# Optimization experiments

Measured on AMD Instinct MI355X. Metric: run time of the kernel, lower is better.

## Reference

```python
import jax, jax.numpy as jnp
import numpy as np

N_NODES = 100000
N_EDGES = 1600000
N_CONCEPTS = 500000
D = 128  # concept_dim = graph_hidden_dim = graph_output_dim


def setup_inputs() -> dict:
    key = jax.random.key(0)
    ks = jax.random.split(key, 10)
    cncpt_ids = jax.random.randint(ks[0], (N_NODES,), 0, N_CONCEPTS)
    src = jax.random.randint(ks[1], (N_EDGES,), 0, N_NODES)
    dst = jax.random.randint(ks[2], (N_EDGES,), 0, N_NODES)
    emb_table = jax.random.normal(ks[3], (N_CONCEPTS, D), dtype=jnp.float32)
    W1 = jax.random.normal(ks[4], (D, D), dtype=jnp.float32) * 0.05
    b1 = jax.random.normal(ks[5], (D,), dtype=jnp.float32) * 0.05
    W2 = jax.random.normal(ks[6], (D, D), dtype=jnp.float32) * 0.05
    b2 = jax.random.normal(ks[7], (D,), dtype=jnp.float32) * 0.05
    Wout = jax.random.normal(ks[8], (1, D), dtype=jnp.float32) * 0.05
    bout = jax.random.normal(ks[9], (1,), dtype=jnp.float32) * 0.05
    return {"cncpt_ids": cncpt_ids, "src": src, "dst": dst,
            "emb_table": emb_table, "W1": W1, "b1": b1,
            "W2": W2, "b2": b2, "Wout": Wout, "bout": bout}


def _gcn_layer(h, src, dst, W, b, n_nodes):
    # DGL update_all(copy_src, sum): gather messages from src, sum into dst
    agg = jax.ops.segment_sum(h[src], dst, num_segments=n_nodes)  # [N, d_in]
    return jax.nn.relu(agg @ W.T + b)  # NodeApplyModule: Linear + ReLU


def reference(cncpt_ids, src, dst, emb_table, W1, b1, W2, b2, Wout, bout):
    n_nodes = cncpt_ids.shape[0]
    h = emb_table[cncpt_ids]                       # [N, D] concept embeddings
    h = _gcn_layer(h, src, dst, W1, b1, n_nodes)   # gcn1
    h = _gcn_layer(h, src, dst, W2, b2, n_nodes)   # gcn2
    x = h[None]                                    # torch.stack([h]) -> [1, N, D]
    logits = jax.nn.sigmoid(x @ Wout.T + bout)     # hidden2output -> [1, N, 1]
    return logits
```

## Files before the change

### kernel.cpp

```cpp
#include <hip/hip_runtime.h>
#include <math.h>

#define D 128
#define SCAN_B 256

typedef __attribute__((ext_vector_type(8))) short bfrag;
typedef __attribute__((ext_vector_type(4))) float ffrag;

__device__ inline unsigned short f2bf(float f) {
    unsigned u = __float_as_uint(f);
    u += 0x7FFF + ((u >> 16) & 1);
    return (unsigned short)(u >> 16);
}
__device__ inline float bf2f(unsigned short h) {
    return __uint_as_float(((unsigned)h) << 16);
}
__device__ inline unsigned pack_bf2(float a, float b) {
    return ((unsigned)f2bf(a)) | (((unsigned)f2bf(b)) << 16);
}

__global__ void zero_int_kernel(int* __restrict__ buf, int n) {
    int i = blockIdx.x * blockDim.x + threadIdx.x;
    if (i < n) buf[i] = 0;
}

__global__ void wsplit_kernel(const float* __restrict__ W1,
                              const float* __restrict__ W2,
                              unsigned short* __restrict__ hi1,
                              unsigned short* __restrict__ lo1,
                              unsigned short* __restrict__ hi2,
                              unsigned short* __restrict__ lo2, int n) {
    int i = blockIdx.x * blockDim.x + threadIdx.x;
    if (i >= n) return;
    float f1 = W1[i];
    unsigned short h1 = f2bf(f1);
    hi1[i] = h1;
    lo1[i] = f2bf(f1 - bf2f(h1));
    float f2 = W2[i];
    unsigned short h2 = f2bf(f2);
    hi2[i] = h2;
    lo2[i] = f2bf(f2 - bf2f(h2));
}

__global__ void gather_kernel(const float* __restrict__ emb,
                              const int* __restrict__ ids,
                              uint4* __restrict__ h4, int n_nodes) {
    int idx = blockIdx.x * blockDim.x + threadIdx.x;
    int total = n_nodes * 16;
    if (idx >= total) return;
    int node = idx >> 4;
    int c = idx & 15;
    size_t cid = (size_t)ids[node];
    const float4* s = (const float4*)(emb + cid * D) + c * 2;
    float4 v0 = s[0];
    float4 v1 = s[1];
    uint4 p;
    p.x = pack_bf2(v0.x, v0.y);
    p.y = pack_bf2(v0.z, v0.w);
    p.z = pack_bf2(v1.x, v1.y);
    p.w = pack_bf2(v1.z, v1.w);
    h4[(size_t)node * 16 + c] = p;
}

__global__ void degree_kernel(const int* __restrict__ dst,
                              int* __restrict__ deg, int n_edges) {
    int e = blockIdx.x * blockDim.x + threadIdx.x;
    if (e < n_edges) atomicAdd(&deg[dst[e]], 1);
}

__global__ __launch_bounds__(SCAN_B) void scan_block_kernel(
        const int* __restrict__ deg, int* __restrict__ row_ptr,
        int* __restrict__ blocksums, int n) {
    __shared__ int s[SCAN_B];
    int i = blockIdx.x * SCAN_B + threadIdx.x;
    int v = (i < n) ? deg[i] : 0;
    s[threadIdx.x] = v;
    __syncthreads();
    #pragma unroll
    for (int off = 1; off < SCAN_B; off <<= 1) {
        int t = (threadIdx.x >= off) ? s[threadIdx.x - off] : 0;
        __syncthreads();
        s[threadIdx.x] += t;
        __syncthreads();
    }
    if (i < n) row_ptr[i] = s[threadIdx.x] - v;
    if (threadIdx.x == SCAN_B - 1) blocksums[blockIdx.x] = s[SCAN_B - 1];
}

__global__ __launch_bounds__(512) void scan_sums_kernel(int* __restrict__ blocksums,
                                                        int nb) {
    __shared__ int s[512];
    int v = (threadIdx.x < nb) ? blocksums[threadIdx.x] : 0;
    s[threadIdx.x] = v;
    __syncthreads();
    #pragma unroll
    for (int off = 1; off < 512; off <<= 1) {
        int t = (threadIdx.x >= off) ? s[threadIdx.x - off] : 0;
        __syncthreads();
        s[threadIdx.x] += t;
        __syncthreads();
    }
    if (threadIdx.x < nb) blocksums[threadIdx.x] = s[threadIdx.x] - v;
}

__global__ void add_offsets_kernel(int* __restrict__ row_ptr,
                                   const int* __restrict__ blocksums,
                                   int* __restrict__ cursor, int n, int n_nodes) {
    int i = blockIdx.x * blockDim.x + threadIdx.x;
    if (i >= n) return;
    int rp = row_ptr[i] + blocksums[i / SCAN_B];
    row_ptr[i] = rp;
    if (i < n_nodes) cursor[i] = rp;
}

__global__ void csr_fill_kernel(const int* __restrict__ src,
                                const int* __restrict__ dst,
                                int* __restrict__ cursor,
                                int* __restrict__ esrc, int n_edges) {
    int e = blockIdx.x * blockDim.x + threadIdx.x;
    if (e >= n_edges) return;
    int pos = atomicAdd(&cursor[dst[e]], 1);
    esrc[pos] = src[e];
}

__global__ __launch_bounds__(256) void agg_kernel(
        const uint4* __restrict__ h4, const int* __restrict__ row_ptr,
        const int* __restrict__ esrc, uint4* __restrict__ agg4, int n_nodes) {
    int node = blockIdx.x * 4 + (threadIdx.x >> 6);
    int lane = threadIdx.x & 63;
    if (node >= n_nodes) return;
    const int c = lane & 15;
    const int g = lane >> 4;
    int beg = row_ptr[node], end = row_ptr[node + 1];

    float a0 = 0.f, a1 = 0.f, a2 = 0.f, a3 = 0.f;
    float a4 = 0.f, a5 = 0.f, a6 = 0.f, a7 = 0.f;

    int i = beg + g;
    for (; i + 4 < end; i += 8) {
        int s0 = esrc[i];
        int s1 = esrc[i + 4];
        uint4 u0 = h4[(size_t)s0 * 16 + c];
        uint4 u1 = h4[(size_t)s1 * 16 + c];
        a0 += __uint_as_float(u0.x << 16) + __uint_as_float(u1.x << 16);
        a1 += __uint_as_float(u0.x & 0xffff0000u) + __uint_as_float(u1.x & 0xffff0000u);
        a2 += __uint_as_float(u0.y << 16) + __uint_as_float(u1.y << 16);
        a3 += __uint_as_float(u0.y & 0xffff0000u) + __uint_as_float(u1.y & 0xffff0000u);
        a4 += __uint_as_float(u0.z << 16) + __uint_as_float(u1.z << 16);
        a5 += __uint_as_float(u0.z & 0xffff0000u) + __uint_as_float(u1.z & 0xffff0000u);
        a6 += __uint_as_float(u0.w << 16) + __uint_as_float(u1.w << 16);
        a7 += __uint_as_float(u0.w & 0xffff0000u) + __uint_as_float(u1.w & 0xffff0000u);
    }
    if (i < end) {
        uint4 u = h4[(size_t)esrc[i] * 16 + c];
        a0 += __uint_as_float(u.x << 16);
        a1 += __uint_as_float(u.x & 0xffff0000u);
        a2 += __uint_as_float(u.y << 16);
        a3 += __uint_as_float(u.y & 0xffff0000u);
        a4 += __uint_as_float(u.z << 16);
        a5 += __uint_as_float(u.z & 0xffff0000u);
        a6 += __uint_as_float(u.w << 16);
        a7 += __uint_as_float(u.w & 0xffff0000u);
    }

    a0 += __shfl_xor(a0, 16, 64); a0 += __shfl_xor(a0, 32, 64);
    a1 += __shfl_xor(a1, 16, 64); a1 += __shfl_xor(a1, 32, 64);
    a2 += __shfl_xor(a2, 16, 64); a2 += __shfl_xor(a2, 32, 64);
    a3 += __shfl_xor(a3, 16, 64); a3 += __shfl_xor(a3, 32, 64);
    a4 += __shfl_xor(a4, 16, 64); a4 += __shfl_xor(a4, 32, 64);
    a5 += __shfl_xor(a5, 16, 64); a5 += __shfl_xor(a5, 32, 64);
    a6 += __shfl_xor(a6, 16, 64); a6 += __shfl_xor(a6, 32, 64);
    a7 += __shfl_xor(a7, 16, 64); a7 += __shfl_xor(a7, 32, 64);

    if (g == 0) {
        uint4 r;
        r.x = pack_bf2(a0, a1);
        r.y = pack_bf2(a2, a3);
        r.z = pack_bf2(a4, a5);
        r.w = pack_bf2(a6, a7);
        agg4[(size_t)node * 16 + c] = r;
    }
}

__global__ __launch_bounds__(256) void linear_mfma_kernel(
        const unsigned short* __restrict__ x,
        const unsigned short* __restrict__ Whi,
        const unsigned short* __restrict__ Wlo,
        const float* __restrict__ b,
        unsigned short* __restrict__ y,
        const float* __restrict__ wout,
        const float* __restrict__ bout,
        float* __restrict__ outp,
        int n_nodes, int fuse_out) {
    const int lane = threadIdx.x & 63;
    const int col  = lane & 15;
    const int quad = lane >> 4;
    const int wave = blockIdx.x * 4 + (threadIdx.x >> 6);
    const int nwaves = gridDim.x * 4;
    const int ngroups = (n_nodes + 15) >> 4;

    float bvals[8], wvals[8];
    #pragma unroll
    for (int nt = 0; nt < 8; ++nt) {
        bvals[nt] = b[nt * 16 + col];
        wvals[nt] = fuse_out ? wout[nt * 16 + col] : 0.f;
    }
    const float bout0 = fuse_out ? bout[0] : 0.f;

    for (int g = wave; g < ngroups; g += nwaves) {
        int node = g * 16 + col;
        int nload = node < n_nodes ? node : (n_nodes - 1);

        bfrag a[4];
        #pragma unroll
        for (int kt = 0; kt < 4; ++kt)
            a[kt] = *(const bfrag*)(x + (size_t)nload * D + kt * 32 + quad * 8);

        const size_t bbase = (size_t)col * D + quad * 8;
        float part0 = 0.f, part1 = 0.f, part2 = 0.f, part3 = 0.f;

        #pragma unroll
        for (int nt = 0; nt < 8; ++nt) {
            ffrag c = {0.f, 0.f, 0.f, 0.f};
            #pragma unroll
            for (int kt = 0; kt < 4; ++kt) {
                size_t off = (size_t)nt * 16 * D + bbase + kt * 32;
                bfrag bh = *(const bfrag*)(Whi + off);
                bfrag bl = *(const bfrag*)(Wlo + off);
                c = __builtin_amdgcn_mfma_f32_16x16x32_bf16(a[kt], bh, c, 0, 0, 0);
                c = __builtin_amdgcn_mfma_f32_16x16x32_bf16(a[kt], bl, c, 0, 0, 0);
            }
            if (fuse_out) {
                part0 += fmaxf(c[0] + bvals[nt], 0.f) * wvals[nt];
                part1 += fmaxf(c[1] + bvals[nt], 0.f) * wvals[nt];
                part2 += fmaxf(c[2] + bvals[nt], 0.f) * wvals[nt];
                part3 += fmaxf(c[3] + bvals[nt], 0.f) * wvals[nt];
            } else {
                #pragma unroll
                for (int r = 0; r < 4; ++r) {
                    int onode = g * 16 + quad * 4 + r;
                    if (onode < n_nodes)
                        y[(size_t)onode * D + nt * 16 + col] =
                            f2bf(fmaxf(c[r] + bvals[nt], 0.f));
                }
            }
        }

        if (fuse_out) {
            float part[4] = {part0, part1, part2, part3};
            #pragma unroll
            for (int r = 0; r < 4; ++r) {
                float s = part[r];
                s += __shfl_xor(s, 1, 64);
                s += __shfl_xor(s, 2, 64);
                s += __shfl_xor(s, 4, 64);
                s += __shfl_xor(s, 8, 64);
                int onode = g * 16 + quad * 4 + r;
                if (col == 0 && onode < n_nodes)
                    outp[onode] = 1.0f / (1.0f + expf(-(s + bout0)));
            }
        }
    }
}

extern "C" void kernel_launch(void* const* d_in, const int* in_sizes, int n_in,
                              void* d_out, int out_size, void* d_ws, size_t ws_size,
                              hipStream_t stream) {
    const int*   cncpt_ids = (const int*)d_in[0];
    const int*   src       = (const int*)d_in[1];
    const int*   dst       = (const int*)d_in[2];
    const float* emb       = (const float*)d_in[3];
    const float* W1        = (const float*)d_in[4];
    const float* b1        = (const float*)d_in[5];
    const float* W2        = (const float*)d_in[6];
    const float* b2        = (const float*)d_in[7];
    const float* Wout      = (const float*)d_in[8];
    const float* bout      = (const float*)d_in[9];
    float* out = (float*)d_out;

    const int n_nodes = in_sizes[0];
    const int n_edges = in_sizes[1];

    unsigned short* bufA = (unsigned short*)d_ws;
    unsigned short* bufB = bufA + (size_t)n_nodes * D;
    int*   deg      = (int*)(bufB + (size_t)n_nodes * D);
    int*   row_ptr  = deg + (n_nodes + 1);
    int*   cursor   = row_ptr + (n_nodes + 1);
    int*   blocksums= cursor + n_nodes;
    int*   esrc     = blocksums + 512;
    unsigned short* W1hi = (unsigned short*)(esrc + n_edges);
    unsigned short* W1lo = W1hi + D * D;
    unsigned short* W2hi = W1lo + D * D;
    unsigned short* W2lo = W2hi + D * D;

    const int np1 = n_nodes + 1;
    const int nb_scan = (np1 + SCAN_B - 1) / SCAN_B;

    wsplit_kernel<<<(D * D + 255) / 256, 256, 0, stream>>>(
        W1, W2, W1hi, W1lo, W2hi, W2lo, D * D);

    gather_kernel<<<(n_nodes * 16 + 255) / 256, 256, 0, stream>>>(
        emb, cncpt_ids, (uint4*)bufA, n_nodes);

    zero_int_kernel<<<(np1 + 255) / 256, 256, 0, stream>>>(deg, np1);
    degree_kernel<<<(n_edges + 255) / 256, 256, 0, stream>>>(dst, deg, n_edges);
    scan_block_kernel<<<nb_scan, SCAN_B, 0, stream>>>(deg, row_ptr, blocksums, np1);
    scan_sums_kernel<<<1, 512, 0, stream>>>(blocksums, nb_scan);
    add_offsets_kernel<<<(np1 + 255) / 256, 256, 0, stream>>>(
        row_ptr, blocksums, cursor, np1, n_nodes);
    csr_fill_kernel<<<(n_edges + 255) / 256, 256, 0, stream>>>(
        src, dst, cursor, esrc, n_edges);

    const int agg_grid = (n_nodes + 3) / 4;
    const int ngroups = (n_nodes + 15) / 16;
    const int lin_grid = (ngroups + 7) / 8;

    agg_kernel<<<agg_grid, 256, 0, stream>>>(
        (const uint4*)bufA, row_ptr, esrc, (uint4*)bufB, n_nodes);
    linear_mfma_kernel<<<lin_grid, 256, 0, stream>>>(
        bufB, W1hi, W1lo, b1, bufA, nullptr, nullptr, nullptr, n_nodes, 0);

    agg_kernel<<<agg_grid, 256, 0, stream>>>(
        (const uint4*)bufA, row_ptr, esrc, (uint4*)bufB, n_nodes);
    linear_mfma_kernel<<<lin_grid, 256, 0, stream>>>(
        bufB, W2hi, W2lo, b2, nullptr, Wout, bout, out, n_nodes, 1);
}
```

Before: 727.2 us.

## Merge setup kernels, prefetch edge indices via shuffle, stage weights in LDS

Combines the weight-split and degree-zeroing launches, and the embedding gather and degree count, into two kernels. This cuts launch count and lets independent work share one grid. The aggregation kernel now loads up to 64 neighbor indices in one coalesced read and broadcasts them with shuffles, so four feature rows are in flight per lane group. The linear kernel copies the hi/lo bf16 weights into padded shared memory once per block instead of reading them from global memory per fragment. This raises LDS use per block, which may lower occupancy.

```diff
diff --git a/kernel.cpp b/kernel.cpp
--- a/kernel.cpp
+++ b/kernel.cpp
@@ -19,53 +19,57 @@
     return ((unsigned)f2bf(a)) | (((unsigned)f2bf(b)) << 16);
 }
 
-__global__ void zero_int_kernel(int* __restrict__ buf, int n) {
-    int i = blockIdx.x * blockDim.x + threadIdx.x;
-    if (i < n) buf[i] = 0;
-}
-
-__global__ void wsplit_kernel(const float* __restrict__ W1,
+__global__ void setup1_kernel(const float* __restrict__ W1,
                               const float* __restrict__ W2,
                               unsigned short* __restrict__ hi1,
                               unsigned short* __restrict__ lo1,
                               unsigned short* __restrict__ hi2,
-                              unsigned short* __restrict__ lo2, int n) {
-    int i = blockIdx.x * blockDim.x + threadIdx.x;
-    if (i >= n) return;
-    float f1 = W1[i];
-    unsigned short h1 = f2bf(f1);
-    hi1[i] = h1;
-    lo1[i] = f2bf(f1 - bf2f(h1));
-    float f2 = W2[i];
-    unsigned short h2 = f2bf(f2);
-    hi2[i] = h2;
-    lo2[i] = f2bf(f2 - bf2f(h2));
-}
-
-__global__ void gather_kernel(const float* __restrict__ emb,
+                              unsigned short* __restrict__ lo2,
+                              int* __restrict__ deg, int np1, int nblk_w) {
+    if ((int)blockIdx.x < nblk_w) {
+        int i = blockIdx.x * blockDim.x + threadIdx.x;
+        if (i < D * D) {
+            float f1 = W1[i];
+            unsigned short h1 = f2bf(f1);
+            hi1[i] = h1;
+            lo1[i] = f2bf(f1 - bf2f(h1));
+            float f2 = W2[i];
+            unsigned short h2 = f2bf(f2);
+            hi2[i] = h2;
+            lo2[i] = f2bf(f2 - bf2f(h2));
+        }
+    } else {
+        int i = ((int)blockIdx.x - nblk_w) * blockDim.x + threadIdx.x;
+        if (i < np1) deg[i] = 0;
+    }
+}
+
+__global__ void setup2_kernel(const float* __restrict__ emb,
                               const int* __restrict__ ids,
-                              uint4* __restrict__ h4, int n_nodes) {
-    int idx = blockIdx.x * blockDim.x + threadIdx.x;
-    int total = n_nodes * 16;
-    if (idx >= total) return;
-    int node = idx >> 4;
-    int c = idx & 15;
-    size_t cid = (size_t)ids[node];
-    const float4* s = (const float4*)(emb + cid * D) + c * 2;
-    float4 v0 = s[0];
-    float4 v1 = s[1];
-    uint4 p;
-    p.x = pack_bf2(v0.x, v0.y);
-    p.y = pack_bf2(v0.z, v0.w);
-    p.z = pack_bf2(v1.x, v1.y);
-    p.w = pack_bf2(v1.z, v1.w);
-    h4[(size_t)node * 16 + c] = p;
-}
-
-__global__ void degree_kernel(const int* __restrict__ dst,
-                              int* __restrict__ deg, int n_edges) {
-    int e = blockIdx.x * blockDim.x + threadIdx.x;
-    if (e < n_edges) atomicAdd(&deg[dst[e]], 1);
+                              uint4* __restrict__ h4,
+                              const int* __restrict__ dst,
+                              int* __restrict__ deg,
+                              int n_nodes, int n_edges, int nblk_g) {
+    if ((int)blockIdx.x < nblk_g) {
+        int idx = blockIdx.x * blockDim.x + threadIdx.x;
+        int total = n_nodes * 16;
+        if (idx >= total) return;
+        int node = idx >> 4;
+        int c = idx & 15;
+        size_t cid = (size_t)ids[node];
+        const float4* s = (const float4*)(emb + cid * D) + c * 2;
+        float4 v0 = s[0];
+        float4 v1 = s[1];
+        uint4 p;
+        p.x = pack_bf2(v0.x, v0.y);
+        p.y = pack_bf2(v0.z, v0.w);
+        p.z = pack_bf2(v1.x, v1.y);
+        p.w = pack_bf2(v1.z, v1.w);
+        h4[(size_t)node * 16 + c] = p;
+    } else {
+        int e = ((int)blockIdx.x - nblk_g) * blockDim.x + threadIdx.x;
+        if (e < n_edges) atomicAdd(&deg[dst[e]], 1);
+    }
 }
 
 __global__ __launch_bounds__(SCAN_B) void scan_block_kernel(
@@ -123,6 +127,13 @@
     esrc[pos] = src[e];
 }
 
+#define ACC8(u) do { \
+    a0 += __uint_as_float((u).x << 16); a1 += __uint_as_float((u).x & 0xffff0000u); \
+    a2 += __uint_as_float((u).y << 16); a3 += __uint_as_float((u).y & 0xffff0000u); \
+    a4 += __uint_as_float((u).z << 16); a5 += __uint_as_float((u).z & 0xffff0000u); \
+    a6 += __uint_as_float((u).w << 16); a7 += __uint_as_float((u).w & 0xffff0000u); \
+} while (0)
+
 __global__ __launch_bounds__(256) void agg_kernel(
         const uint4* __restrict__ h4, const int* __restrict__ row_ptr,
         const int* __restrict__ esrc, uint4* __restrict__ agg4, int n_nodes) {
@@ -132,35 +143,38 @@
     const int c = lane & 15;
     const int g = lane >> 4;
     int beg = row_ptr[node], end = row_ptr[node + 1];
+    int deg = end - beg;
+
+    int myidx = 0;
+    if (lane < deg) myidx = esrc[beg + lane];
 
     float a0 = 0.f, a1 = 0.f, a2 = 0.f, a3 = 0.f;
     float a4 = 0.f, a5 = 0.f, a6 = 0.f, a7 = 0.f;
 
-    int i = beg + g;
-    for (; i + 4 < end; i += 8) {
-        int s0 = esrc[i];
-        int s1 = esrc[i + 4];
-        uint4 u0 = h4[(size_t)s0 * 16 + c];
-        uint4 u1 = h4[(size_t)s1 * 16 + c];
-        a0 += __uint_as_float(u0.x << 16) + __uint_as_float(u1.x << 16);
-        a1 += __uint_as_float(u0.x & 0xffff0000u) + __uint_as_float(u1.x & 0xffff0000u);
-        a2 += __uint_as_float(u0.y << 16) + __uint_as_float(u1.y << 16);
-        a3 += __uint_as_float(u0.y & 0xffff0000u) + __uint_as_float(u1.y & 0xffff0000u);
-        a4 += __uint_as_float(u0.z << 16) + __uint_as_float(u1.z << 16);
-        a5 += __uint_as_float(u0.z & 0xffff0000u) + __uint_as_float(u1.z & 0xffff0000u);
-        a6 += __uint_as_float(u0.w << 16) + __uint_as_float(u1.w << 16);
-        a7 += __uint_as_float(u0.w & 0xffff0000u) + __uint_as_float(u1.w & 0xffff0000u);
-    }
-    if (i < end) {
+    int nfast = deg < 64 ? deg : 64;
+    for (int base = 0; base < nfast; base += 16) {
+        int p0 = base + g;
+        int s0 = __shfl(myidx, p0, 64);
+        int s1 = __shfl(myidx, p0 + 4, 64);
+        int s2 = __shfl(myidx, p0 + 8, 64);
+        int s3 = __shfl(myidx, p0 + 12, 64);
+        bool v0 = p0 < nfast;
+        bool v1 = (p0 + 4) < nfast;
+        bool v2 = (p0 + 8) < nfast;
+        bool v3 = (p0 + 12) < nfast;
+        uint4 u0, u1, u2, u3;
+        if (v0) u0 = h4[(size_t)s0 * 16 + c];
+        if (v1) u1 = h4[(size_t)s1 * 16 + c];
+        if (v2) u2 = h4[(size_t)s2 * 16 + c];
+        if (v3) u3 = h4[(size_t)s3 * 16 + c];
+        if (v0) ACC8(u0);
+        if (v1) ACC8(u1);
+        if (v2) ACC8(u2);
+        if (v3) ACC8(u3);
+    }
+    for (int i = beg + 64 + g; i < end; i += 4) {
         uint4 u = h4[(size_t)esrc[i] * 16 + c];
-        a0 += __uint_as_float(u.x << 16);
-        a1 += __uint_as_float(u.x & 0xffff0000u);
-        a2 += __uint_as_float(u.y << 16);
-        a3 += __uint_as_float(u.y & 0xffff0000u);
-        a4 += __uint_as_float(u.z << 16);
-        a5 += __uint_as_float(u.z & 0xffff0000u);
-        a6 += __uint_as_float(u.w << 16);
-        a7 += __uint_as_float(u.w & 0xffff0000u);
+        ACC8(u);
     }
 
     a0 += __shfl_xor(a0, 16, 64); a0 += __shfl_xor(a0, 32, 64);
@@ -192,6 +206,21 @@
         const float* __restrict__ bout,
         float* __restrict__ outp,
         int n_nodes, int fuse_out) {
+    __shared__ __align__(16) unsigned short sW[2][D][136];
+
+    {
+        const uint4* Wh4 = (const uint4*)Whi;
+        const uint4* Wl4 = (const uint4*)Wlo;
+        #pragma unroll
+        for (int j = 0; j < 8; ++j) {
+            int ch = (int)threadIdx.x + j * 256;
+            int row = ch >> 4, k8 = ch & 15;
+            *(uint4*)&sW[0][row][k8 * 8] = Wh4[ch];
+            *(uint4*)&sW[1][row][k8 * 8] = Wl4[ch];
+        }
+    }
+    __syncthreads();
+
     const int lane = threadIdx.x & 63;
     const int col  = lane & 15;
     const int quad = lane >> 4;
@@ -216,7 +245,6 @@
         for (int kt = 0; kt < 4; ++kt)
             a[kt] = *(const bfrag*)(x + (size_t)nload * D + kt * 32 + quad * 8);
 
-        const size_t bbase = (size_t)col * D + quad * 8;
         float part0 = 0.f, part1 = 0.f, part2 = 0.f, part3 = 0.f;
 
         #pragma unroll
@@ -224,9 +252,8 @@
             ffrag c = {0.f, 0.f, 0.f, 0.f};
             #pragma unroll
             for (int kt = 0; kt < 4; ++kt) {
-                size_t off = (size_t)nt * 16 * D + bbase + kt * 32;
-                bfrag bh = *(const bfrag*)(Whi + off);
-                bfrag bl = *(const bfrag*)(Wlo + off);
+                bfrag bh = *(const bfrag*)&sW[0][nt * 16 + col][kt * 32 + quad * 8];
+                bfrag bl = *(const bfrag*)&sW[1][nt * 16 + col][kt * 32 + quad * 8];
                 c = __builtin_amdgcn_mfma_f32_16x16x32_bf16(a[kt], bh, c, 0, 0, 0);
                 c = __builtin_amdgcn_mfma_f32_16x16x32_bf16(a[kt], bl, c, 0, 0, 0);
             }
@@ -288,7 +315,8 @@
     int*   cursor   = row_ptr + (n_nodes + 1);
     int*   blocksums= cursor + n_nodes;
     int*   esrc     = blocksums + 512;
-    unsigned short* W1hi = (unsigned short*)(esrc + n_edges);
+    size_t walign   = ((size_t)(esrc + n_edges) + 15) & ~(size_t)15;
+    unsigned short* W1hi = (unsigned short*)walign;
     unsigned short* W1lo = W1hi + D * D;
     unsigned short* W2hi = W1lo + D * D;
     unsigned short* W2lo = W2hi + D * D;
@@ -296,20 +324,21 @@
     const int np1 = n_nodes + 1;
     const int nb_scan = (np1 + SCAN_B - 1) / SCAN_B;
 
-    wsplit_kernel<<<(D * D + 255) / 256, 256, 0, stream>>>(
-        W1, W2, W1hi, W1lo, W2hi, W2lo, D * D);
-
-    gather_kernel<<<(n_nodes * 16 + 255) / 256, 256, 0, stream>>>(
-        emb, cncpt_ids, (uint4*)bufA, n_nodes);
-
-    zero_int_kernel<<<(np1 + 255) / 256, 256, 0, stream>>>(deg, np1);
-    degree_kernel<<<(n_edges + 255) / 256, 256, 0, stream>>>(dst, deg, n_edges);
+    const int nblk_w = (D * D + 255) / 256;
+    const int nblk_z = (np1 + 255) / 256;
+    setup1_kernel<<<nblk_w + nblk_z, 256, 0, stream>>>(
+        W1, W2, W1hi, W1lo, W2hi, W2lo, deg, np1, nblk_w);
+
+    const int nblk_g = (n_nodes * 16 + 255) / 256;
+    const int nblk_d = (n_edges + 255) / 256;
+    setup2_kernel<<<nblk_g + nblk_d, 256, 0, stream>>>(
+        emb, cncpt_ids, (uint4*)bufA, dst, deg, n_nodes, n_edges, nblk_g);
+
     scan_block_kernel<<<nb_scan, SCAN_B, 0, stream>>>(deg, row_ptr, blocksums, np1);
     scan_sums_kernel<<<1, 512, 0, stream>>>(blocksums, nb_scan);
     add_offsets_kernel<<<(np1 + 255) / 256, 256, 0, stream>>>(
         row_ptr, blocksums, cursor, np1, n_nodes);
-    csr_fill_kernel<<<(n_edges + 255) / 256, 256, 0, stream>>>(
-        src, dst, cursor, esrc, n_edges);
+    csr_fill_kernel<<<nblk_d, 256, 0, stream>>>(src, dst, cursor, esrc, n_edges);
 
     const int agg_grid = (n_nodes + 3) / 4;
     const int ngroups = (n_nodes + 15) / 16;
```

After: 674.3 us. 1.08x faster.
